# Kernel optimization log

Measured on AMD Instinct MI355X. Metric: run time of the kernel, lower is better.

## Reference

```python
import jax, jax.numpy as jnp
import numpy as np

D_MODEL = 1024
D_STATE = 64
N_HEADS = 16
CHUNK = 64


def segsum(x):
    # x: (..., T) -> (..., T, T) with [i, j] = sum_{j<k<=i} x[k], -inf above diagonal
    T = x.shape[-1]
    xx = jnp.broadcast_to(x[..., None], x.shape + (T,))  # [i, j] = x[i]
    lower = jnp.tril(jnp.ones((T, T), dtype=bool), -1)
    xs = jnp.cumsum(jnp.where(lower, xx, 0.0), axis=-2)
    keep = jnp.tril(jnp.ones((T, T), dtype=bool), 0)
    return jnp.where(keep, xs, -jnp.inf)


def ssd_minimal(X, A, B, C, block_len):
    b, L, h, p = X.shape
    n = B.shape[-1]
    c = L // block_len
    l = block_len
    X = X.reshape(b, c, l, h, p)
    A = A.reshape(b, c, l, h).transpose(0, 3, 1, 2)  # b h c l
    B = B.reshape(b, c, l, h, n)
    C = C.reshape(b, c, l, h, n)
    A_cumsum = jnp.cumsum(A, axis=-1)  # b h c l
    Lmat = jnp.exp(segsum(A))  # b h c l l
    Y_diag = jnp.einsum('bclhn,bcshn,bhcls,bcshp->bclhp', C, B, Lmat, X)
    decay_states = jnp.exp(A_cumsum[:, :, :, -1:] - A_cumsum)  # b h c l
    states = jnp.einsum('bclhn,bhcl,bclhp->bchpn', B, decay_states, X)
    init = jnp.zeros_like(states[:, :1])
    states = jnp.concatenate([init, states], axis=1)  # b (c+1) h p n
    A_last = A_cumsum[:, :, :, -1]  # b h c
    decay_chunk = jnp.exp(segsum(jnp.pad(A_last, ((0, 0), (0, 0), (1, 0)))))  # b h (c+1) (c+1)
    new_states = jnp.einsum('bhzc,bchpn->bzhpn', decay_chunk, states)
    states, final_state = new_states[:, :-1], new_states[:, -1]
    state_decay_out = jnp.exp(A_cumsum)  # b h c l
    Y_off = jnp.einsum('bclhn,bchpn,bhcl->bclhp', C, states, state_decay_out)
    Y = (Y_diag + Y_off).reshape(b, L, h, p)
    return Y, final_state


def mamba2_forward(x, W_in, W_dt, b_dt, W_B, W_C, W_out, A_log):
    b, L, d = x.shape
    h, n = N_HEADS, D_STATE
    p = d // h
    # seqlen divisible by CHUNK -> no padding needed (pad_len == 0)
    xz = x @ W_in.T  # (b, L, 2d)
    x_in, z = xz[..., :d], xz[..., d:]
    dt = jax.nn.softplus(x @ W_dt.T + b_dt)  # (b, L, h)
    A = -jnp.exp(A_log)[None, None, :] * dt  # (b, L, h)
    B = (x @ W_B.T).reshape(b, L, h, n)
    C = (x @ W_C.T).reshape(b, L, h, n)
    X = x_in.reshape(b, L, h, p) * dt[..., None]
    Y, new_state = ssd_minimal(X, A, B, C, CHUNK)
    y = Y.reshape(b, L, d) * jax.nn.silu(z)
    y = y @ W_out.T
    return y, new_state


def setup_inputs() -> dict:
    key = jax.random.key(0)
    ks = jax.random.split(key, 7)
    d, h, n = D_MODEL, N_HEADS, D_STATE
    x = jax.random.normal(ks[0], (2, 4096, d), dtype=jnp.float32)
    # xavier_uniform with gain 0.5 for in/out proj
    lim_in = 0.5 * np.sqrt(6.0 / (d + 2 * d))
    W_in = jax.random.uniform(ks[1], (2 * d, d), minval=-lim_in, maxval=lim_in, dtype=jnp.float32)
    lim_out = 0.5 * np.sqrt(6.0 / (d + d))
    W_out = jax.random.uniform(ks[2], (d, d), minval=-lim_out, maxval=lim_out, dtype=jnp.float32)
    # default torch Linear init (kaiming-uniform-ish): U(-1/sqrt(fan_in), 1/sqrt(fan_in))
    lim = 1.0 / np.sqrt(d)
    W_dt = jax.random.uniform(ks[3], (h, d), minval=-lim, maxval=lim, dtype=jnp.float32)
    b_dt = jnp.zeros((h,), dtype=jnp.float32)
    W_B = jax.random.uniform(ks[4], (h * n, d), minval=-lim, maxval=lim, dtype=jnp.float32)
    W_C = jax.random.uniform(ks[5], (h * n, d), minval=-lim, maxval=lim, dtype=jnp.float32)
    A_log = jnp.log(jnp.linspace(1.0, 16.0, h)).astype(jnp.float32)
    return {"x": x, "W_in": W_in, "W_dt": W_dt, "b_dt": b_dt, "W_B": W_B, "W_C": W_C, "W_out": W_out, "A_log": A_log}


def reference(x, W_in, W_dt, b_dt, W_B, W_C, W_out, A_log):
    return mamba2_forward(x, W_in, W_dt, b_dt, W_B, W_C, W_out, A_log)
```

## Files before the change

kernel.cpp:

```cpp
#include <hip/hip_runtime.h>
#include <cstdint>
#include <cstddef>

#define NTOK 8192

typedef __bf16 bf16x8 __attribute__((ext_vector_type(8)));
typedef float f32x4 __attribute__((ext_vector_type(4)));
typedef float f32x4v __attribute__((ext_vector_type(4)));
typedef unsigned short u16x8 __attribute__((ext_vector_type(8)));

__device__ __forceinline__ float b2f(unsigned short u) {
    return __uint_as_float(((unsigned int)u) << 16);
}
__device__ __forceinline__ unsigned short f2b(float f) {
    unsigned int u = __float_as_uint(f);
    u += 0x7FFFu + ((u >> 16) & 1u);
    return (unsigned short)(u >> 16);
}

__device__ __forceinline__ void async_lds16(unsigned short* lds, const unsigned short* g) {
    __builtin_amdgcn_global_load_lds(
        (const __attribute__((address_space(1))) unsigned int*)g,
        (__attribute__((address_space(3))) unsigned int*)lds,
        16, 0, 0);
}

template <int N> __device__ __forceinline__ void waitcnt_vm() {
    if constexpr (N == 8)      asm volatile("s_waitcnt vmcnt(8)" ::: "memory");
    else if constexpr (N == 6) asm volatile("s_waitcnt vmcnt(6)" ::: "memory");
    else if constexpr (N == 4) asm volatile("s_waitcnt vmcnt(4)" ::: "memory");
    else if constexpr (N == 3) asm volatile("s_waitcnt vmcnt(3)" ::: "memory");
    else                       asm volatile("s_waitcnt vmcnt(0)" ::: "memory");
}

__global__ __launch_bounds__(256) void prep(
    const float* __restrict__ x, const float* __restrict__ W_in,
    const float* __restrict__ W_B, const float* __restrict__ W_C,
    unsigned short* __restrict__ xb, unsigned short* __restrict__ Wst,
    const float* __restrict__ s16a, const float* __restrict__ s16b,
    float* __restrict__ alogf, float* __restrict__ bdtf)
{
    const long i = (long)blockIdx.x * 256 + threadIdx.x;
    const float* src; unsigned short* dst; long off;
    if (i < 1048576)      { src = x;    dst = xb;            off = i; }
    else if (i < 1310720) { src = W_in; dst = Wst;           off = i - 1048576; }
    else if (i < 1441792) { src = W_B;  dst = Wst + 2097152; off = i - 1310720; }
    else if (i < 1572864) { src = W_C;  dst = Wst + 3145728; off = i - 1441792; }
    else {
        if (i == 1572864) {
            float ma = 0.f, mb = 0.f;
            for (int k = 0; k < 16; k++) { ma = fmaxf(ma, fabsf(s16a[k])); mb = fmaxf(mb, fabsf(s16b[k])); }
            const float* alog = (ma >= mb) ? s16a : s16b;
            const float* bdt  = (ma >= mb) ? s16b : s16a;
            for (int k = 0; k < 16; k++) { alogf[k] = alog[k]; bdtf[k] = bdt[k]; }
        }
        return;
    }
    const f32x4v* p = (const f32x4v*)(src + off * 8);
    f32x4v a = p[0], b = p[1];
    u16x8 v;
#pragma unroll
    for (int t = 0; t < 4; t++) { v[t] = f2b(a[t]); v[t + 4] = f2b(b[t]); }
    *(u16x8*)(dst + off * 8) = v;
}

__global__ __launch_bounds__(256) void f32_to_bf16(
    const float* __restrict__ in, unsigned short* __restrict__ out, int n8)
{
    const int i = blockIdx.x * 256 + threadIdx.x;
    if (i >= n8) return;
    const f32x4v* p = (const f32x4v*)(in + (long)i * 8);
    f32x4v a = p[0], b = p[1];
    u16x8 v;
#pragma unroll
    for (int t = 0; t < 4; t++) { v[t] = f2b(a[t]); v[t + 4] = f2b(b[t]); }
    *(u16x8*)(out + (long)i * 8) = v;
}

__global__ __launch_bounds__(256) void dt_kernel(
    const float* __restrict__ x, const float* __restrict__ Wdt,
    const float* __restrict__ bdt, const float* __restrict__ Alog,
    float* __restrict__ dtp, float* __restrict__ Ap)
{
    const int token = blockIdx.x * 16 + (threadIdx.x >> 4);
    const int h = threadIdx.x & 15;
    const f32x4v* xr = (const f32x4v*)(x + (long)token * 1024);
    const f32x4v* wr = (const f32x4v*)(Wdt + h * 1024);
    float s0 = bdt[h], s1 = 0.f;
#pragma unroll 8
    for (int k = 0; k < 256; k += 2) {
        f32x4v a0 = xr[k], w0 = wr[k];
        f32x4v a1 = xr[k + 1], w1 = wr[k + 1];
        s0 += a0[0] * w0[0] + a0[1] * w0[1] + a0[2] * w0[2] + a0[3] * w0[3];
        s1 += a1[0] * w1[0] + a1[1] * w1[1] + a1[2] * w1[2] + a1[3] * w1[3];
    }
    const float s = s0 + s1;
    const float dtv = (s > 15.f) ? s : log1pf(expf(s));
    dtp[token * 16 + h] = dtv;
    Ap[token * 16 + h] = -expf(Alog[h]) * dtv;
}

template <int MODE, int NI>
__global__ __launch_bounds__(512, 2) void gemm256(
    const unsigned short* __restrict__ A, const unsigned short* __restrict__ W,
    const int NT_N, const int N, const int K,
    void* __restrict__ out0, unsigned short* __restrict__ out1,
    unsigned short* __restrict__ out2, unsigned short* __restrict__ out3,
    const float* __restrict__ dtp)
{
    constexpr int BN = NI * 64;
    constexpr int LPT = 2 + NI / 2;

    __shared__ unsigned short As[4][256 * 32];
    __shared__ unsigned short Ws[4][BN * 32];

    const int tid = threadIdx.x;
    const int lane = tid & 63;
    const int warp = tid >> 6;
    const int wm = warp >> 2;
    const int wn = warp & 3;
    const int qm = lane & 15;
    const int quad = lane >> 4;

    const int nwg = gridDim.x;
    const int cpx = nwg >> 3;
    const int bid = blockIdx.x;
    const int swz = (bid & 7) * cpx + (bid >> 3);
    const int bx = swz % NT_N;
    const int by = swz / NT_N;
    const long arow0 = (long)by * 256;
    const long wrow0 = (long)bx * BN;

    const int srow = tid >> 2;
    const int scol = (tid & 3) * 8;

    f32x4 acc[8][NI];
    const f32x4 zero = {0.f, 0.f, 0.f, 0.f};
#pragma unroll
    for (int i = 0; i < 8; i++)
#pragma unroll
        for (int j = 0; j < NI; j++) acc[i][j] = zero;

    auto stage = [&](int buf, int k0) {
#pragma unroll
        for (int i = 0; i < 2; i++)
            async_lds16(As[buf] + i * 4096 + tid * 8,
                        A + (arow0 + i * 128 + srow) * (long)K + k0 + scol);
#pragma unroll
        for (int i = 0; i < NI / 2; i++)
            async_lds16(Ws[buf] + i * 4096 + tid * 8,
                        W + (wrow0 + i * 128 + srow) * (long)K + k0 + scol);
    };
    auto compute = [&](const unsigned short* Ab, const unsigned short* Wb) {
        bf16x8 fa[8], fb[NI];
#pragma unroll
        for (int mi = 0; mi < 8; mi++)
            fa[mi] = *(const bf16x8*)(Ab + (wm * 128 + mi * 16 + qm) * 32 + quad * 8);
#pragma unroll
        for (int ni = 0; ni < NI; ni++)
            fb[ni] = *(const bf16x8*)(Wb + (wn * (NI * 16) + ni * 16 + qm) * 32 + quad * 8);
#pragma unroll
        for (int mi = 0; mi < 8; mi++)
#pragma unroll
            for (int ni = 0; ni < NI; ni++)
                acc[mi][ni] = __builtin_amdgcn_mfma_f32_16x16x32_bf16(
                    fa[mi], fb[ni], acc[mi][ni], 0, 0, 0);
    };

    const int nt = K >> 5;
    stage(0, 0); stage(1, 32); stage(2, 64);
    waitcnt_vm<2 * LPT>(); __builtin_amdgcn_s_barrier();
    int t = 0;
    for (; t < nt - 3; ++t) {
        stage((t + 3) & 3, (t + 3) << 5);
        compute(As[t & 3], Ws[t & 3]);
        waitcnt_vm<2 * LPT>(); __builtin_amdgcn_s_barrier();
    }
    compute(As[t & 3], Ws[t & 3]); waitcnt_vm<LPT>(); __builtin_amdgcn_s_barrier(); ++t;
    compute(As[t & 3], Ws[t & 3]); waitcnt_vm<0>();   __builtin_amdgcn_s_barrier(); ++t;
    compute(As[t & 3], Ws[t & 3]);

#pragma unroll
    for (int mi = 0; mi < 8; mi++)
#pragma unroll
        for (int ni = 0; ni < NI; ni++)
#pragma unroll
            for (int r = 0; r < 4; r++) {
                const long row = arow0 + wm * 128 + mi * 16 + quad * 4 + r;
                const int col = (int)wrow0 + wn * (NI * 16) + ni * 16 + qm;
                const float v = acc[mi][ni][r];
                if (MODE == 0) {
                    ((float*)out0)[row * N + col] = v;
                } else {
                    const int seg = col >> 10, cc = col & 1023;
                    if (seg == 0) {
                        ((unsigned short*)out0)[row * 1024 + cc] = f2b(v * dtp[row * 16 + (cc >> 6)]);
                    } else if (seg == 1) {
                        out1[row * 1024 + cc] = f2b(v / (1.f + expf(-v)));
                    } else if (seg == 2) {
                        out2[row * 1024 + cc] = f2b(v);
                    } else {
                        out3[row * 1024 + cc] = f2b(v);
                    }
                }
            }
}

__global__ __launch_bounds__(256) void ssd_states(
    const unsigned short* __restrict__ Xb, const unsigned short* __restrict__ Bb,
    const float* __restrict__ Ap, float* __restrict__ st_out,
    float* __restrict__ Alast)
{
    __shared__ __align__(16) unsigned short Xh[64 * 64];
    __shared__ __align__(16) unsigned short Xl[64 * 64];
    __shared__ __align__(16) unsigned short Bt[64 * 64];
    __shared__ float Acum[64];
    __shared__ float dec[64];

    const int blk = blockIdx.x;
    const int h = blk & 15;
    const int c = (blk >> 4) & 63;
    const int b = blk >> 10;
    const long tokenbase = (long)b * 4096 + (long)c * 64;
    const int tid = threadIdx.x;
    const int lane = tid & 63;
    const int w = tid >> 6;
    const int qm = lane & 15;
    const int quad = lane >> 4;

    if (tid < 64) Acum[tid] = Ap[(tokenbase + tid) * 16 + h];

    const int row = tid & 63;
    u16x8 rx[2], rb[2];
#pragma unroll
    for (int i = 0; i < 2; i++) {
        const int ch = (tid >> 6) + 4 * i;
        const long g = (tokenbase + row) * 1024 + h * 64 + ch * 8;
        rx[i] = *(const u16x8*)(Xb + g);
        rb[i] = *(const u16x8*)(Bb + g);
    }
    __syncthreads();
    if (tid == 0) {
        float s = 0.f;
        for (int l = 0; l < 64; l++) { s += Acum[l]; Acum[l] = s; }
        Alast[(b * 16 + h) * 64 + c] = s;
    }
    __syncthreads();
    if (tid < 64) dec[tid] = expf(Acum[63] - Acum[tid]);
    __syncthreads();

    const float dv = dec[row];
#pragma unroll
    for (int i = 0; i < 2; i++) {
        const int ch = (tid >> 6) + 4 * i;
#pragma unroll
        for (int t = 0; t < 8; t++) {
            const int pn = ch * 8 + t;
            const int d = (pn * 64 + row) ^ (t << 3);
            const float xd = b2f(rx[i][t]) * dv;
            const unsigned short hi = f2b(xd);
            Xh[d] = hi;
            Xl[d] = f2b(xd - b2f(hi));
            Bt[d] = rb[i][t];
        }
    }
    __syncthreads();

    f32x4 acc[4];
    const f32x4 zero = {0.f, 0.f, 0.f, 0.f};
#pragma unroll
    for (int ni = 0; ni < 4; ni++) acc[ni] = zero;
#pragma unroll
    for (int kk2 = 0; kk2 < 2; kk2++) {
        const int ko = kk2 * 32 + quad * 8;
        const int ra = 16 * w + qm;
        const int da = (ra * 64 + ko) ^ ((ra & 7) << 3);
        bf16x8 fxh = *(const bf16x8*)(Xh + da);
        bf16x8 fxl = *(const bf16x8*)(Xl + da);
#pragma unroll
        for (int ni = 0; ni < 4; ni++) {
            const int rn = ni * 16 + qm;
            bf16x8 fb = *(const bf16x8*)(Bt + ((rn * 64 + ko) ^ ((rn & 7) << 3)));
            acc[ni] = __builtin_amdgcn_mfma_f32_16x16x32_bf16(fxh, fb, acc[ni], 0, 0, 0);
            acc[ni] = __builtin_amdgcn_mfma_f32_16x16x32_bf16(fxl, fb, acc[ni], 0, 0, 0);
        }
    }
    const long sbase = (long)blk * 4096;
    const int p0 = 16 * w + quad * 4;
#pragma unroll
    for (int ni = 0; ni < 4; ni++)
#pragma unroll
        for (int r = 0; r < 4; r++)
            st_out[sbase + (p0 + r) * 64 + ni * 16 + qm] = acc[ni][r];
}

__global__ __launch_bounds__(256) void scan_kernel(
    float* __restrict__ st, const float* __restrict__ Alast)
{
    const int blk = blockIdx.x;
    const int grp = blk & 15;
    const int h = (blk >> 4) & 15;
    const int b = blk >> 8;
    const int e = grp * 256 + threadIdx.x;
    const float* al = Alast + (b * 16 + h) * 64;
    float M = 0.f;
    for (int c = 0; c < 64; c++) {
        const long idx = ((long)((b * 64 + c) * 16 + h)) * 4096 + e;
        const float s = st[idx];
        st[idx] = M;
        M = expf(al[c]) * M + s;
    }
    st[(long)8388608 + (long)(b * 16 + h) * 4096 + e] = M;
}

__global__ __launch_bounds__(256) void ssd_yoff(
    const unsigned short* __restrict__ Xb, const unsigned short* __restrict__ Bb,
    const unsigned short* __restrict__ Cb, const float* __restrict__ Ap,
    const float* __restrict__ st, unsigned short* __restrict__ SZb)
{
    __shared__ __align__(16) unsigned short Bs[64 * 64];
    __shared__ __align__(16) unsigned short Ss[64 * 64];
    __shared__ __align__(16) unsigned short Xt[64 * 64];
    __shared__ __align__(16) unsigned short Gs[64 * 64];
    __shared__ float Acum[64];

    const int blk = blockIdx.x;
    const int h = blk & 15;
    const int c = (blk >> 4) & 63;
    const int b = blk >> 10;
    const long tokenbase = (long)b * 4096 + (long)c * 64;
    const int tid = threadIdx.x;
    const int lane = tid & 63;
    const int w = tid >> 6;
    const int qm = lane & 15;
    const int quad = lane >> 4;
    const long sbase = (long)blk * 4096;

    if (tid < 64) Acum[tid] = Ap[(tokenbase + tid) * 16 + h];

#pragma unroll
    for (int i = 0; i < 2; i++) {
        const int idx = tid + i * 256;
        const int r8 = idx >> 3, c8 = (idx & 7) * 8;
        const long g = (tokenbase + r8) * 1024 + h * 64 + c8;
        const int d = (r8 * 64 + c8) ^ ((r8 & 7) << 3);
        *(u16x8*)(Bs + d) = *(const u16x8*)(Bb + g);
        const float* sp = st + sbase + r8 * 64 + c8;
        f32x4v s0 = *(const f32x4v*)sp, s1 = *(const f32x4v*)(sp + 4);
        u16x8 sv;
#pragma unroll
        for (int t = 0; t < 4; t++) { sv[t] = f2b(s0[t]); sv[t + 4] = f2b(s1[t]); }
        *(u16x8*)(Ss + d) = sv;
    }
    const int xrow = tid & 63;
#pragma unroll
    for (int i = 0; i < 2; i++) {
        const int ch = (tid >> 6) + 4 * i;
        const long g = (tokenbase + xrow) * 1024 + h * 64 + ch * 8;
        u16x8 xv = *(const u16x8*)(Xb + g);
#pragma unroll
        for (int t = 0; t < 8; t++) {
            const int p = ch * 8 + t;
            Xt[(p * 64 + xrow) ^ (t << 3)] = xv[t];
        }
    }
    u16x8 fc[2];
#pragma unroll
    for (int kk2 = 0; kk2 < 2; kk2++)
        fc[kk2] = *(const u16x8*)(Cb + (tokenbase + 16 * w + qm) * 1024 + h * 64 + kk2 * 32 + quad * 8);

    __syncthreads();
    if (tid == 0) {
        float s = 0.f;
        for (int l = 0; l < 64; l++) { s += Acum[l]; Acum[l] = s; }
    }

    f32x4 acc1[4], acc2[4];
    const f32x4 zero = {0.f, 0.f, 0.f, 0.f};
#pragma unroll
    for (int ni = 0; ni < 4; ni++) { acc1[ni] = zero; acc2[ni] = zero; }
#pragma unroll
    for (int kk2 = 0; kk2 < 2; kk2++) {
        const int ko = kk2 * 32 + quad * 8;
        bf16x8 fa = *(const bf16x8*)&fc[kk2];
#pragma unroll
        for (int ni = 0; ni < 4; ni++) {
            const int rn = ni * 16 + qm;
            const int d = (rn * 64 + ko) ^ ((rn & 7) << 3);
            bf16x8 fbb = *(const bf16x8*)(Bs + d);
            acc1[ni] = __builtin_amdgcn_mfma_f32_16x16x32_bf16(fa, fbb, acc1[ni], 0, 0, 0);
            bf16x8 fbs = *(const bf16x8*)(Ss + d);
            acc2[ni] = __builtin_amdgcn_mfma_f32_16x16x32_bf16(fa, fbs, acc2[ni], 0, 0, 0);
        }
    }
    __syncthreads();

    const int l0 = 16 * w + quad * 4;
    float al[4];
#pragma unroll
    for (int r = 0; r < 4; r++) al[r] = Acum[l0 + r];
#pragma unroll
    for (int ni = 0; ni < 4; ni++) {
        const int s = ni * 16 + qm;
        const float as = Acum[s];
#pragma unroll
        for (int r = 0; r < 4; r++) {
            const int l = l0 + r;
            const float gv = (s <= l) ? acc1[ni][r] * expf(al[r] - as) : 0.f;
            Gs[(l * 64 + s) ^ ((l & 7) << 3)] = f2b(gv);
        }
    }
    __syncthreads();

    f32x4 acc3[4];
#pragma unroll
    for (int ni = 0; ni < 4; ni++) acc3[ni] = zero;
#pragma unroll
    for (int kk2 = 0; kk2 < 2; kk2++) {
        const int ko = kk2 * 32 + quad * 8;
        const int ra = 16 * w + qm;
        bf16x8 fg = *(const bf16x8*)(Gs + ((ra * 64 + ko) ^ ((ra & 7) << 3)));
#pragma unroll
        for (int ni = 0; ni < 4; ni++) {
            const int rp = ni * 16 + qm;
            bf16x8 fx = *(const bf16x8*)(Xt + ((rp * 64 + ko) ^ ((rp & 7) << 3)));
            acc3[ni] = __builtin_amdgcn_mfma_f32_16x16x32_bf16(fg, fx, acc3[ni], 0, 0, 0);
        }
    }
    float eds[4];
#pragma unroll
    for (int r = 0; r < 4; r++) eds[r] = expf(al[r]);
#pragma unroll
    for (int ni = 0; ni < 4; ni++) {
#pragma unroll
        for (int r = 0; r < 4; r++) {
            const int l = l0 + r;
            const int p = ni * 16 + qm;
            const float Y = acc3[ni][r] + eds[r] * acc2[ni][r];
            const long o = (tokenbase + l) * 1024 + h * 64 + p;
            SZb[o] = f2b(Y * b2f(SZb[o]));
        }
    }
}

extern "C" void kernel_launch(void* const* d_in, const int* in_sizes, int n_in,
                              void* d_out, int out_size, void* d_ws, size_t ws_size,
                              hipStream_t stream)
{
    int ix = 0, iwin = 1, iwdt = 2, i1m[3] = {4, 5, 6}, n1m = 0, i16[2] = {3, 7}, n16 = 0;
    for (int i = 0; i < n_in; i++) {
        switch (in_sizes[i]) {
            case 8388608: ix = i; break;
            case 2097152: iwin = i; break;
            case 16384:   iwdt = i; break;
            case 1048576: if (n1m < 3) i1m[n1m++] = i; break;
            case 16:      if (n16 < 2) i16[n16++] = i; break;
            default: break;
        }
    }
    if (n1m < 3) { i1m[0] = 4; i1m[1] = 5; i1m[2] = 6; }
    if (n16 < 2) { i16[0] = 3; i16[1] = 7; }
    const float* x     = (const float*)d_in[ix];
    const float* W_in  = (const float*)d_in[iwin];
    const float* W_dt  = (const float*)d_in[iwdt];
    const float* W_B   = (const float*)d_in[i1m[0]];
    const float* W_C   = (const float*)d_in[i1m[1]];
    const float* W_out = (const float*)d_in[i1m[2]];
    const float* s16a  = (const float*)d_in[i16[0]];
    const float* s16b  = (const float*)d_in[i16[1]];
    float* out = (float*)d_out;

    char* ws = (char*)d_ws;
    float* dtp   = (float*)(ws);
    float* Ap    = (float*)(ws + 524288);
    float* Alast = (float*)(ws + 1048576);
    float* Alogf = (float*)(ws + 1056768);
    float* bdtf  = (float*)(ws + 1056832);
    unsigned short* Xb  = (unsigned short*)(ws + 2097152);
    unsigned short* Bb  = (unsigned short*)(ws + 18874368);
    unsigned short* Cb  = (unsigned short*)(ws + 35651584);
    unsigned short* SZb = (unsigned short*)(ws + 52428800);

    unsigned short* xb  = (unsigned short*)d_out;
    unsigned short* Wst = (unsigned short*)((char*)d_out + 16777216);
    unsigned short* Wob = Xb;

    float* states = out;

    prep<<<6145, 256, 0, stream>>>(x, W_in, W_B, W_C, xb, Wst, s16a, s16b, Alogf, bdtf);
    dt_kernel<<<NTOK / 16, 256, 0, stream>>>(x, W_dt, bdtf, Alogf, dtp, Ap);
    gemm256<1, 4><<<512, 512, 0, stream>>>(xb, Wst, 16, 4096, 1024, Xb, SZb, Bb, Cb, dtp);
    ssd_states<<<2048, 256, 0, stream>>>(Xb, Bb, Ap, states, Alast);
    scan_kernel<<<512, 256, 0, stream>>>(states, Alast);
    ssd_yoff<<<2048, 256, 0, stream>>>(Xb, Bb, Cb, Ap, states, SZb);
    f32_to_bf16<<<512, 256, 0, stream>>>(W_out, Wob, 131072);
    gemm256<0, 2><<<256, 512, 0, stream>>>(SZb, Wob, 8, 1024, 1024, out, nullptr, nullptr, nullptr, nullptr);
}
```

Measured before the change: 404.3 us.

## Use double-buffered BK64 swizzled GEMM pipeline and warp-shuffle chunk cumsums

The GEMM main loop changes from a 4-stage, 32-wide-K async pipeline with manual vmcnt waits to a 2-stage, 64-wide-K double buffer. LDS addresses get an XOR swizzle to avoid bank conflicts, and synchronisation uses plain __syncthreads. Separately, the serial single-thread cumsum of A in ssd_states and ssd_yoff becomes a 64-lane shuffle scan, which also drops a barrier. The scan kernel now precomputes exp(Alast) in shared memory instead of calling expf inside the loop. The shallower prefetch depth may expose more memory latency in the GEMM, traded against fewer barriers and conflict-free fragment loads.

```diff
diff --git a/kernel.cpp b/kernel.cpp
--- a/kernel.cpp
+++ b/kernel.cpp
@@ -23,14 +23,6 @@
         (const __attribute__((address_space(1))) unsigned int*)g,
         (__attribute__((address_space(3))) unsigned int*)lds,
         16, 0, 0);
-}
-
-template <int N> __device__ __forceinline__ void waitcnt_vm() {
-    if constexpr (N == 8)      asm volatile("s_waitcnt vmcnt(8)" ::: "memory");
-    else if constexpr (N == 6) asm volatile("s_waitcnt vmcnt(6)" ::: "memory");
-    else if constexpr (N == 4) asm volatile("s_waitcnt vmcnt(4)" ::: "memory");
-    else if constexpr (N == 3) asm volatile("s_waitcnt vmcnt(3)" ::: "memory");
-    else                       asm volatile("s_waitcnt vmcnt(0)" ::: "memory");
 }
 
 __global__ __launch_bounds__(256) void prep(
@@ -109,10 +101,9 @@
     const float* __restrict__ dtp)
 {
     constexpr int BN = NI * 64;
-    constexpr int LPT = 2 + NI / 2;
-
-    __shared__ unsigned short As[4][256 * 32];
-    __shared__ unsigned short Ws[4][BN * 32];
+
+    __shared__ unsigned short As[2][256 * 64];
+    __shared__ unsigned short Ws[2][BN * 64];
 
     const int tid = threadIdx.x;
     const int lane = tid & 63;
@@ -131,8 +122,8 @@
     const long arow0 = (long)by * 256;
     const long wrow0 = (long)bx * BN;
 
-    const int srow = tid >> 2;
-    const int scol = (tid & 3) * 8;
+    const int srow = tid >> 3;
+    const int sgc = ((tid & 7) ^ (srow & 7)) * 8;
 
     f32x4 acc[8][NI];
     const f32x4 zero = {0.f, 0.f, 0.f, 0.f};
@@ -143,42 +134,49 @@
 
     auto stage = [&](int buf, int k0) {
 #pragma unroll
-        for (int i = 0; i < 2; i++)
-            async_lds16(As[buf] + i * 4096 + tid * 8,
-                        A + (arow0 + i * 128 + srow) * (long)K + k0 + scol);
-#pragma unroll
-        for (int i = 0; i < NI / 2; i++)
-            async_lds16(Ws[buf] + i * 4096 + tid * 8,
-                        W + (wrow0 + i * 128 + srow) * (long)K + k0 + scol);
+        for (int r = 0; r < 4; r++)
+            async_lds16(As[buf] + r * 4096 + tid * 8,
+                        A + (arow0 + r * 64 + srow) * (long)K + k0 + sgc);
+#pragma unroll
+        for (int r = 0; r < NI; r++)
+            async_lds16(Ws[buf] + r * 4096 + tid * 8,
+                        W + (wrow0 + r * 64 + srow) * (long)K + k0 + sgc);
     };
+    const int rx = (qm & 7) << 3;
     auto compute = [&](const unsigned short* Ab, const unsigned short* Wb) {
-        bf16x8 fa[8], fb[NI];
-#pragma unroll
-        for (int mi = 0; mi < 8; mi++)
-            fa[mi] = *(const bf16x8*)(Ab + (wm * 128 + mi * 16 + qm) * 32 + quad * 8);
-#pragma unroll
-        for (int ni = 0; ni < NI; ni++)
-            fb[ni] = *(const bf16x8*)(Wb + (wn * (NI * 16) + ni * 16 + qm) * 32 + quad * 8);
-#pragma unroll
-        for (int mi = 0; mi < 8; mi++)
-#pragma unroll
-            for (int ni = 0; ni < NI; ni++)
-                acc[mi][ni] = __builtin_amdgcn_mfma_f32_16x16x32_bf16(
-                    fa[mi], fb[ni], acc[mi][ni], 0, 0, 0);
+#pragma unroll
+        for (int kk = 0; kk < 64; kk += 32) {
+            bf16x8 fa[8], fb[NI];
+#pragma unroll
+            for (int mi = 0; mi < 8; mi++) {
+                const int row = wm * 128 + mi * 16 + qm;
+                fa[mi] = *(const bf16x8*)(Ab + ((row * 64 + kk + quad * 8) ^ rx));
+            }
+#pragma unroll
+            for (int ni = 0; ni < NI; ni++) {
+                const int row = wn * (NI * 16) + ni * 16 + qm;
+                fb[ni] = *(const bf16x8*)(Wb + ((row * 64 + kk + quad * 8) ^ rx));
+            }
+#pragma unroll
+            for (int mi = 0; mi < 8; mi++)
+#pragma unroll
+                for (int ni = 0; ni < NI; ni++)
+                    acc[mi][ni] = __builtin_amdgcn_mfma_f32_16x16x32_bf16(
+                        fa[mi], fb[ni], acc[mi][ni], 0, 0, 0);
+        }
     };
 
-    const int nt = K >> 5;
-    stage(0, 0); stage(1, 32); stage(2, 64);
-    waitcnt_vm<2 * LPT>(); __builtin_amdgcn_s_barrier();
-    int t = 0;
-    for (; t < nt - 3; ++t) {
-        stage((t + 3) & 3, (t + 3) << 5);
-        compute(As[t & 3], Ws[t & 3]);
-        waitcnt_vm<2 * LPT>(); __builtin_amdgcn_s_barrier();
-    }
-    compute(As[t & 3], Ws[t & 3]); waitcnt_vm<LPT>(); __builtin_amdgcn_s_barrier(); ++t;
-    compute(As[t & 3], Ws[t & 3]); waitcnt_vm<0>();   __builtin_amdgcn_s_barrier(); ++t;
-    compute(As[t & 3], Ws[t & 3]);
+    const int nk = K >> 6;
+    int cur = 0;
+    stage(0, 0);
+    __syncthreads();
+    for (int t = 1; t < nk; t++) {
+        stage(cur ^ 1, t << 6);
+        compute(As[cur], Ws[cur]);
+        __syncthreads();
+        cur ^= 1;
+    }
+    compute(As[cur], Ws[cur]);
 
 #pragma unroll
     for (int mi = 0; mi < 8; mi++)
@@ -214,7 +212,6 @@
     __shared__ __align__(16) unsigned short Xh[64 * 64];
     __shared__ __align__(16) unsigned short Xl[64 * 64];
     __shared__ __align__(16) unsigned short Bt[64 * 64];
-    __shared__ float Acum[64];
     __shared__ float dec[64];
 
     const int blk = blockIdx.x;
@@ -228,8 +225,6 @@
     const int qm = lane & 15;
     const int quad = lane >> 4;
 
-    if (tid < 64) Acum[tid] = Ap[(tokenbase + tid) * 16 + h];
-
     const int row = tid & 63;
     u16x8 rx[2], rb[2];
 #pragma unroll
@@ -239,14 +234,17 @@
         rx[i] = *(const u16x8*)(Xb + g);
         rb[i] = *(const u16x8*)(Bb + g);
     }
-    __syncthreads();
-    if (tid == 0) {
-        float s = 0.f;
-        for (int l = 0; l < 64; l++) { s += Acum[l]; Acum[l] = s; }
-        Alast[(b * 16 + h) * 64 + c] = s;
-    }
-    __syncthreads();
-    if (tid < 64) dec[tid] = expf(Acum[63] - Acum[tid]);
+    if (tid < 64) {
+        float v = Ap[(tokenbase + tid) * 16 + h];
+#pragma unroll
+        for (int off = 1; off < 64; off <<= 1) {
+            const float u = __shfl_up(v, off, 64);
+            if (tid >= off) v += u;
+        }
+        const float tot = __shfl(v, 63, 64);
+        dec[tid] = expf(tot - v);
+        if (tid == 63) Alast[(b * 16 + h) * 64 + c] = v;
+    }
     __syncthreads();
 
     const float dv = dec[row];
@@ -297,18 +295,21 @@
 __global__ __launch_bounds__(256) void scan_kernel(
     float* __restrict__ st, const float* __restrict__ Alast)
 {
+    __shared__ float eal[64];
     const int blk = blockIdx.x;
     const int grp = blk & 15;
     const int h = (blk >> 4) & 15;
     const int b = blk >> 8;
     const int e = grp * 256 + threadIdx.x;
     const float* al = Alast + (b * 16 + h) * 64;
+    if (threadIdx.x < 64) eal[threadIdx.x] = expf(al[threadIdx.x]);
+    __syncthreads();
     float M = 0.f;
     for (int c = 0; c < 64; c++) {
         const long idx = ((long)((b * 64 + c) * 16 + h)) * 4096 + e;
         const float s = st[idx];
         st[idx] = M;
-        M = expf(al[c]) * M + s;
+        M = eal[c] * M + s;
     }
     st[(long)8388608 + (long)(b * 16 + h) * 4096 + e] = M;
 }
@@ -336,7 +337,15 @@
     const int quad = lane >> 4;
     const long sbase = (long)blk * 4096;
 
-    if (tid < 64) Acum[tid] = Ap[(tokenbase + tid) * 16 + h];
+    if (tid < 64) {
+        float v = Ap[(tokenbase + tid) * 16 + h];
+#pragma unroll
+        for (int off = 1; off < 64; off <<= 1) {
+            const float u = __shfl_up(v, off, 64);
+            if (tid >= off) v += u;
+        }
+        Acum[tid] = v;
+    }
 
 #pragma unroll
     for (int i = 0; i < 2; i++) {
@@ -370,10 +379,6 @@
         fc[kk2] = *(const u16x8*)(Cb + (tokenbase + 16 * w + qm) * 1024 + h * 64 + kk2 * 32 + quad * 8);
 
     __syncthreads();
-    if (tid == 0) {
-        float s = 0.f;
-        for (int l = 0; l < 64; l++) { s += Acum[l]; Acum[l] = s; }
-    }
 
     f32x4 acc1[4], acc2[4];
     const f32x4 zero = {0.f, 0.f, 0.f, 0.f};
@@ -393,7 +398,6 @@
             acc2[ni] = __builtin_amdgcn_mfma_f32_16x16x32_bf16(fa, fbs, acc2[ni], 0, 0, 0);
         }
     }
-    __syncthreads();
 
     const int l0 = 16 * w + quad * 4;
     float al[4];
```

Result: faster. 366.7 us (-9.3%).
